# Performance work log

Measured on AMD Instinct MI355X. Metric: run time of the kernel, lower is better.

## Reference

```python
import jax, jax.numpy as jnp
import numpy as np
from jax import lax

K_NBR = 9  # K nearest neighbors
R = 2      # shuffle_scale


def pixel_unshuffle(x, r):
    B, C, H, W = x.shape
    x = x.reshape(B, C, H // r, r, W // r, r)
    return x.transpose(0, 1, 3, 5, 2, 4).reshape(B, C * r * r, H // r, W // r)


def pixel_shuffle(x, r):
    B, C, H, W = x.shape
    x = x.reshape(B, C // (r * r), r, r, H, W)
    return x.transpose(0, 1, 4, 2, 5, 3).reshape(B, C // (r * r), H * r, W * r)


def conv2d_same(x, w, b):
    y = lax.conv_general_dilated(x, w, (1, 1), 'SAME',
                                 dimension_numbers=('NCHW', 'OIHW', 'NCHW'))
    return y + b[None, :, None, None]


def convnn_branching_layer(x, idx, wa, ba, wb, bb, wp, bp):
    """Conv2d_ConvNN_Random_Branching with shuffle_pattern='BA'."""
    x = pixel_unshuffle(x, R)                      # (B, C*r^2, H/r, W/r)
    B, C, H, W = x.shape
    T = H * W
    # Branch 1: standard 3x3 conv
    y1 = conv2d_same(x, wa, ba)                    # (B, c1, H, W)
    # Branch 2: ConvNN on K nearest of N random samples
    xt = x.reshape(B, C, T)                        # tokens
    samp = xt[:, :, idx]                           # (B, C, N) random samples
    dots = jnp.einsum('bct,bcn->btn', xt, samp)
    xn = jnp.sum(xt * xt, axis=1)[:, :, None]      # (B, T, 1)
    sn = jnp.sum(samp * samp, axis=1)[:, None, :]  # (B, 1, N)
    dist = xn + sn - 2.0 * dots                    # squared euclidean (B, T, N)
    nbr = lax.top_k(-dist, K_NBR)[1]               # (B, T, K) indices into samples
    # gather neighbor features: (B, C, T*K)
    g = jnp.take_along_axis(samp, nbr.reshape(B, 1, T * K_NBR), axis=2)
    g = g.reshape(B, C, T, K_NBR)
    # Conv1d(kernel=K, stride=K) over stacked neighbors
    y2 = jnp.einsum('bctk,ock->bot', g, wb) + bb[None, :, None]
    y2 = y2.reshape(B, wb.shape[0], H, W)          # (B, c2, H, W)
    y = jax.nn.relu(jnp.concatenate([y1, y2], axis=1))
    y = conv2d_same(y, wp, bp)                     # 1x1 -> out*r^2 channels
    return pixel_shuffle(y, R)                     # (B, out, H*r, W*r)


def setup_inputs() -> dict:
    key = jax.random.key(0)
    ks = jax.random.split(key, 24)
    s = 0.02
    B = 256
    inp = {
        'x': jax.random.normal(ks[0], (B, 3, 32, 32), jnp.float32),
        'idx1': jax.random.randint(ks[1], (64,), 0, 256, jnp.int32),
        'idx2': jax.random.randint(ks[2], (64,), 0, 256, jnp.int32),
        # layer 1: Cin = 3*4 = 12, branches 16+16, out 16*4 = 64 pre-shuffle
        'w1a': jax.random.normal(ks[3], (16, 12, 3, 3), jnp.float32) * s,
        'b1a': jnp.zeros((16,), jnp.float32),
        'w1b': jax.random.normal(ks[4], (16, 12, 9), jnp.float32) * s,
        'b1b': jnp.zeros((16,), jnp.float32),
        'w1p': jax.random.normal(ks[5], (64, 32, 1, 1), jnp.float32) * s,
        'b1p': jnp.zeros((64,), jnp.float32),
        # layer 2: Cin = 16*4 = 64, branches 32+32, out 32*4 = 128 pre-shuffle
        'w2a': jax.random.normal(ks[6], (32, 64, 3, 3), jnp.float32) * s,
        'b2a': jnp.zeros((32,), jnp.float32),
        'w2b': jax.random.normal(ks[7], (32, 64, 9), jnp.float32) * s,
        'b2b': jnp.zeros((32,), jnp.float32),
        'w2p': jax.random.normal(ks[8], (128, 64, 1, 1), jnp.float32) * s,
        'b2p': jnp.zeros((128,), jnp.float32),
        # FC head
        'fc1w': jax.random.normal(ks[9], (1024, 32768), jnp.float32) * s,
        'fc1b': jnp.zeros((1024,), jnp.float32),
        'fc2w': jax.random.normal(ks[10], (10, 1024), jnp.float32) * s,
        'fc2b': jnp.zeros((10,), jnp.float32),
    }
    return inp


def reference(x, idx1, idx2, w1a, b1a, w1b, b1b, w1p, b1p,
              w2a, b2a, w2b, b2b, w2p, b2p, fc1w, fc1b, fc2w, fc2b):
    h = convnn_branching_layer(x, idx1, w1a, b1a, w1b, b1b, w1p, b1p)  # (B,16,32,32)
    h = convnn_branching_layer(h, idx2, w2a, b2a, w2b, b2b, w2p, b2p)  # (B,32,32,32)
    h = h.reshape(h.shape[0], -1)                   # (B, 32768)
    h = jax.nn.relu(h @ fc1w.T + fc1b)
    return h @ fc2w.T + fc2b                        # (B, num_classes)
```

## Files before the change

### kernel.cpp

```cpp
#include <hip/hip_runtime.h>
#include <cstdint>
#include <cstddef>


#define DI static __device__ __forceinline__

typedef __attribute__((ext_vector_type(8))) short short8;
typedef __attribute__((ext_vector_type(4))) float f32x4;

DI unsigned short f2bf(float v) {
  return __builtin_bit_cast(unsigned short, (__bf16)v);
}
DI float bf2f(unsigned short h) {
  return (float)__builtin_bit_cast(__bf16, h);
}

DI float xu1_at(const float* __restrict__ x, int b, int c, int t) {
  int h = t >> 4, w = t & 15;
  return x[(((size_t)b * 3 + (c >> 2)) * 32 + 2 * h + ((c >> 1) & 1)) * 32 + 2 * w + (c & 1)];
}

__global__ __launch_bounds__(256) void k_prepw(
    const float* __restrict__ w1b, float* __restrict__ wT1,
    const float* __restrict__ w2b, float* __restrict__ wT2,
    const float* __restrict__ w1p, float* __restrict__ wp1T,
    const float* __restrict__ w2p, float* __restrict__ wp2T,
    const float* __restrict__ w1a, float* __restrict__ wa1T,
    const float* __restrict__ w2a, float* __restrict__ wa2T)
{
  int i = blockIdx.x * 256 + threadIdx.x;
  if (i < 1728) {
    int k = i / 192, r = i % 192, c = r >> 4, o = r & 15;
    wT1[i] = w1b[((size_t)o * 12 + c) * 9 + k];
    return;
  }
  i -= 1728;
  if (i < 18432) {
    int k = i / 2048, r = i % 2048, c = r >> 5, o = r & 31;
    wT2[i] = w2b[((size_t)o * 64 + c) * 9 + k];
    return;
  }
  i -= 18432;
  if (i < 2048) { int ic = i >> 6, o = i & 63; wp1T[i] = w1p[(size_t)o * 32 + ic]; return; }
  i -= 2048;
  if (i < 8192) { int ic = i >> 7, o = i & 127; wp2T[i] = w2p[(size_t)o * 64 + ic]; return; }
  i -= 8192;
  if (i < 1728) {
    int o = i & 15, u = i >> 4, ic = u / 9, tp = u % 9;
    wa1T[i] = w1a[((size_t)o * 12 + ic) * 9 + tp];
    return;
  }
  i -= 1728;
  if (i < 18432) {
    int o = i & 31, u = i >> 5, ic = u / 9, tp = u % 9;
    wa2T[i] = w2a[((size_t)o * 64 + ic) * 9 + tp];
  }
}

template <int CIN, bool GATHER, int CCTOT, int OCT>
__global__ __launch_bounds__(256) void k_conv3x3(
    const float* __restrict__ xsrc, const float* __restrict__ xu,
    const float* __restrict__ waT, const float* __restrict__ bias,
    float* __restrict__ ycat)
{
  int b = blockIdx.x;
  int ocb = blockIdx.y * 16;
  __shared__ float xs[CIN * 256];
  int t = threadIdx.x;
  if (GATHER) {
    for (int i = t; i < CIN * 256; i += 256) {
      int c = i >> 8, tt = i & 255;
      xs[i] = xu1_at(xsrc, b, c, tt);
    }
  } else {
    for (int i = t; i < CIN * 256; i += 256) xs[i] = xu[(size_t)b * CIN * 256 + i];
  }
  __syncthreads();
  int tt = t & 127, og = t >> 7;
  int oc0 = ocb + og * 8;
  int h0 = tt >> 4, wc = tt & 15;
  float acc0[8], acc1[8];
#pragma unroll
  for (int o = 0; o < 8; ++o) { acc0[o] = bias[oc0 + o]; acc1[o] = acc0[o]; }
  bool vw0 = wc > 0, vw2 = wc < 15, vh0 = h0 > 0, vh7 = h0 < 7;
  bool m0v[9] = {vh0 && vw0, vh0, vh0 && vw2, vw0, true, vw2, vw0, true, vw2};
  bool m1v[9] = {vw0, true, vw2, vw0, true, vw2, vh7 && vw0, vh7, vh7 && vw2};
  int tc0[9], tc1[9];
#pragma unroll
  for (int dh = 0; dh < 3; ++dh)
#pragma unroll
    for (int dw = 0; dw < 3; ++dw) {
      int o0 = (h0 + dh - 1) * 16 + (wc + dw - 1);
      int o1 = (h0 + 8 + dh - 1) * 16 + (wc + dw - 1);
      tc0[dh * 3 + dw] = o0 < 0 ? 0 : (o0 > 255 ? 255 : o0);
      tc1[dh * 3 + dw] = o1 < 0 ? 0 : (o1 > 255 ? 255 : o1);
    }
#pragma unroll 2
  for (int ic = 0; ic < CIN; ++ic) {
    float xv0[9], xv1[9];
#pragma unroll
    for (int tp = 0; tp < 9; ++tp) {
      float v0 = xs[ic * 256 + tc0[tp]];
      float v1 = xs[ic * 256 + tc1[tp]];
      xv0[tp] = m0v[tp] ? v0 : 0.f;
      xv1[tp] = m1v[tp] ? v1 : 0.f;
    }
#pragma unroll
    for (int tp = 0; tp < 9; ++tp) {
      const float* wp = waT + ((size_t)ic * 9 + tp) * OCT + oc0;
      float4 wA = *(const float4*)wp;
      float4 wB = *(const float4*)(wp + 4);
      float wv[8] = {wA.x, wA.y, wA.z, wA.w, wB.x, wB.y, wB.z, wB.w};
#pragma unroll
      for (int o = 0; o < 8; ++o) {
        acc0[o] = fmaf(xv0[tp], wv[o], acc0[o]);
        acc1[o] = fmaf(xv1[tp], wv[o], acc1[o]);
      }
    }
  }
#pragma unroll
  for (int o = 0; o < 8; ++o) {
    ycat[((size_t)b * CCTOT + oc0 + o) * 256 + tt] = fmaxf(acc0[o], 0.f);
    ycat[((size_t)b * CCTOT + oc0 + o) * 256 + tt + 128] = fmaxf(acc1[o], 0.f);
  }
}

template <int C, int STR, bool GATHER>
__global__ __launch_bounds__(256) void k_prep(
    const float* __restrict__ xsrc, const float* __restrict__ xu,
    const int* __restrict__ idx,
    float* __restrict__ sampT, float* __restrict__ samp_cn,
    float* __restrict__ snvg)
{
  int b = blockIdx.x, t = threadIdx.x;
  __shared__ float sph[C * 64];
  __shared__ int idxs[64];
  if (t < 64) idxs[t] = idx[t];
  __syncthreads();
  for (int i = t; i < C * 64; i += 256) {
    int c = i >> 6, n = i & 63;
    int p = idxs[n];
    sph[i] = GATHER ? xu1_at(xsrc, b, c, p) : xu[((size_t)b * C + c) * 256 + p];
  }
  __syncthreads();
  for (int i = t; i < C * 64; i += 256) samp_cn[(size_t)b * C * 64 + i] = sph[i];
  for (int i = t; i < 64 * STR; i += 256) {
    int n = i / STR, c = i % STR;
    if (c < C) sampT[(size_t)b * 64 * STR + i] = sph[c * 64 + n];
  }
  if (t < 64) {
    float s;
    {
#pragma clang fp contract(off)
      s = 0.f;
      for (int c = 0; c < C; ++c) { float v = sph[c * 64 + t]; s += v * v; }
    }
    snvg[(size_t)b * 64 + t] = s;
  }
}

template <int C, int STR, bool GATHER>
__global__ __launch_bounds__(256) void k_nbr(
    const float* __restrict__ xsrc, const float* __restrict__ xu,
    const float* __restrict__ sampT, const float* __restrict__ snvg,
    int* __restrict__ nbr)
{
  int b = blockIdx.x, t = threadIdx.x;
  float xcol[C];
#pragma unroll
  for (int c = 0; c < C; ++c)
    xcol[c] = GATHER ? xu1_at(xsrc, b, c, t) : xu[((size_t)b * C + c) * 256 + t];
  float xn;
  {
#pragma clang fp contract(off)
    xn = 0.f;
#pragma unroll
    for (int c = 0; c < C; ++c) xn += xcol[c] * xcol[c];
  }
  float bd[9];
  int bn[9];
#pragma unroll
  for (int i = 0; i < 9; ++i) { bd[i] = __builtin_inff(); bn[i] = 1 << 30; }

#pragma unroll 1
  for (int n = 0; n < 64; ++n) {
    const float* sp = sampT + ((size_t)b * 64 + n) * STR;
    float snvn = snvg[(size_t)b * 64 + n];
    float d;
    {
#pragma clang fp contract(off)
      float dot = 0.f;
#pragma unroll
      for (int c = 0; c < C; ++c) dot = fmaf(xcol[c], sp[c], dot);
      d = (xn + snvn) - 2.f * dot;
    }
    if (d < bd[8] || (d == bd[8] && n < bn[8])) {
      float dc = d;
      int nc = n;
#pragma unroll
      for (int i = 0; i < 9; ++i) {
        bool sw = (dc < bd[i]) || (dc == bd[i] && nc < bn[i]);
        float ob = bd[i]; int on = bn[i];
        bd[i] = sw ? dc : ob; bn[i] = sw ? nc : on;
        dc = sw ? ob : dc;   nc = sw ? on : nc;
      }
    }
  }
#pragma unroll
  for (int k = 0; k < 9; ++k) nbr[((size_t)b * 9 + k) * 256 + t] = bn[k];
}

template <int C, int OPT, int OTOT, int CCTOT, int OCBASE>
__global__ __launch_bounds__(256) void k_einsum(
    const float* __restrict__ samp_cn,
    const int* __restrict__ nbr,
    const float* __restrict__ wT,
    const float* __restrict__ bb,
    float* __restrict__ ycat)
{
  int b = blockIdx.x, t = threadIdx.x;
  int tt = t & 127, og = t >> 7;
  int o0 = og * OPT;
  __shared__ float samps[C * 64];
  for (int i = t; i < C * 64; i += 256)
    samps[i] = samp_cn[(size_t)b * C * 64 + i];
  int bnA[9], bnB[9];
#pragma unroll
  for (int k = 0; k < 9; ++k) {
    bnA[k] = nbr[((size_t)b * 9 + k) * 256 + tt];
    bnB[k] = nbr[((size_t)b * 9 + k) * 256 + tt + 128];
  }
  __syncthreads();
  float acc0[OPT], acc1[OPT];
#pragma unroll
  for (int o = 0; o < OPT; ++o) { acc0[o] = bb[o0 + o]; acc1[o] = acc0[o]; }
#pragma unroll 1
  for (int k = 0; k < 9; ++k) {
    int n0 = bnA[k], n1 = bnB[k];
#pragma unroll 2
    for (int c = 0; c < C; ++c) {
      float sv0 = samps[c * 64 + n0];
      float sv1 = samps[c * 64 + n1];
      const float* wp = wT + ((size_t)k * C + c) * OTOT + o0;
#pragma unroll
      for (int oq = 0; oq < OPT / 4; ++oq) {
        float4 wv = ((const float4*)wp)[oq];
        float w4[4] = {wv.x, wv.y, wv.z, wv.w};
#pragma unroll
        for (int j = 0; j < 4; ++j) {
          acc0[oq * 4 + j] = fmaf(sv0, w4[j], acc0[oq * 4 + j]);
          acc1[oq * 4 + j] = fmaf(sv1, w4[j], acc1[oq * 4 + j]);
        }
      }
    }
  }
#pragma unroll
  for (int o = 0; o < OPT; ++o) {
    ycat[((size_t)b * CCTOT + OCBASE + o0 + o) * 256 + tt] = fmaxf(acc0[o], 0.f);
    ycat[((size_t)b * CCTOT + OCBASE + o0 + o) * 256 + tt + 128] = fmaxf(acc1[o], 0.f);
  }
}

template <int CIN, int OPT, int OCTOT, bool SHUF>
__global__ __launch_bounds__(256) void k_conv1x1(
    const float* __restrict__ yin, const float* __restrict__ wpT,
    const float* __restrict__ bias, float* __restrict__ out)
{
  int b = blockIdx.x, ocb = blockIdx.y * 2 * OPT, t = threadIdx.x;
  int tt = t & 127, og = t >> 7;
  int o0 = ocb + og * OPT;
  __shared__ float ys[CIN * 256];
  for (int i = t; i < CIN * 256; i += 256) ys[i] = yin[(size_t)b * CIN * 256 + i];
  __syncthreads();
  float acc0[OPT], acc1[OPT];
#pragma unroll
  for (int o = 0; o < OPT; ++o) { acc0[o] = bias[o0 + o]; acc1[o] = acc0[o]; }
#pragma unroll 2
  for (int ic = 0; ic < CIN; ++ic) {
    float sv0 = ys[ic * 256 + tt];
    float sv1 = ys[ic * 256 + tt + 128];
    const float* wp = wpT + (size_t)ic * OCTOT + o0;
#pragma unroll
    for (int oq = 0; oq < OPT / 4; ++oq) {
      float4 wv = ((const float4*)wp)[oq];
      float w4[4] = {wv.x, wv.y, wv.z, wv.w};
#pragma unroll
      for (int j = 0; j < 4; ++j) {
        acc0[oq * 4 + j] = fmaf(sv0, w4[j], acc0[oq * 4 + j]);
        acc1[oq * 4 + j] = fmaf(sv1, w4[j], acc1[oq * 4 + j]);
      }
    }
  }
  int h0 = tt >> 4, wc = tt & 15;
#pragma unroll
  for (int o = 0; o < OPT; ++o) {
    int ogl = o0 + o;
    if (SHUF) {
      int f0 = (ogl >> 2) * 1024 + (2 * h0 + ((ogl >> 1) & 1)) * 32 + (2 * wc + (ogl & 1));
      int f1 = (ogl >> 2) * 1024 + (2 * (h0 + 8) + ((ogl >> 1) & 1)) * 32 + (2 * wc + (ogl & 1));
      out[(size_t)b * 32768 + f0] = acc0[o];
      out[(size_t)b * 32768 + f1] = acc1[o];
    } else {
      out[((size_t)b * OCTOT + ogl) * 256 + tt] = acc0[o];
      out[((size_t)b * OCTOT + ogl) * 256 + tt + 128] = acc1[o];
    }
  }
}

__global__ __launch_bounds__(256, 2) void k_fc1(
    const float* __restrict__ A, const float* __restrict__ W,
    float* __restrict__ parts)
{
  constexpr int KTOT = 32768;
  constexpr int LDT = 36;
  __shared__ unsigned short Ah[128 * LDT], Am[128 * LDT], Al[128 * LDT];
  int t = threadIdx.x;
  int nb = blockIdx.x, mb = blockIdx.y, sb = blockIdx.z;
  int m0 = mb * 128, n0 = nb * 128, k0 = sb * 1024;
  int wave = t >> 6, lane = t & 63;
  int q = lane >> 4, m16 = lane & 15;

  f32x4 acc[8][2];
#pragma unroll
  for (int mt = 0; mt < 8; ++mt)
#pragma unroll
    for (int nt = 0; nt < 2; ++nt) acc[mt][nt] = (f32x4){0.f, 0.f, 0.f, 0.f};

  int arow = t >> 1, acol = (t & 1) * 16;
  const float* Ap = A + (size_t)(m0 + arow) * KTOT + k0 + acol;
  const float* W0 = W + (size_t)(n0 + wave * 32 + m16) * KTOT + k0 + q * 8;
  const float* W1 = W + (size_t)(n0 + wave * 32 + 16 + m16) * KTOT + k0 + q * 8;

  float4 aR0 = *(const float4*)(Ap + 0);
  float4 aR1 = *(const float4*)(Ap + 4);
  float4 aR2 = *(const float4*)(Ap + 8);
  float4 aR3 = *(const float4*)(Ap + 12);
  float4 w0a = *(const float4*)(W0), w0b = *(const float4*)(W0 + 4);
  float4 w1a = *(const float4*)(W1), w1b = *(const float4*)(W1 + 4);

  for (int ks = 0; ks < 1024; ks += 32) {
    int ksn = (ks + 32 < 1024) ? ks + 32 : 0;
    float4 nA0 = *(const float4*)(Ap + ksn);
    float4 nA1 = *(const float4*)(Ap + ksn + 4);
    float4 nA2 = *(const float4*)(Ap + ksn + 8);
    float4 nA3 = *(const float4*)(Ap + ksn + 12);
    float4 nW0a = *(const float4*)(W0 + ksn), nW0b = *(const float4*)(W0 + ksn + 4);
    float4 nW1a = *(const float4*)(W1 + ksn), nW1b = *(const float4*)(W1 + ksn + 4);

    short8 bh[2], bm[2], bl[2];
    {
      float wf0[8] = {w0a.x, w0a.y, w0a.z, w0a.w, w0b.x, w0b.y, w0b.z, w0b.w};
      float wf1[8] = {w1a.x, w1a.y, w1a.z, w1a.w, w1b.x, w1b.y, w1b.z, w1b.w};
#pragma unroll
      for (int j = 0; j < 8; ++j) {
        unsigned short h = f2bf(wf0[j]); float r1 = wf0[j] - bf2f(h);
        unsigned short m = f2bf(r1);
        bh[0][j] = (short)h; bm[0][j] = (short)m; bl[0][j] = (short)f2bf(r1 - bf2f(m));
        h = f2bf(wf1[j]); r1 = wf1[j] - bf2f(h);
        m = f2bf(r1);
        bh[1][j] = (short)h; bm[1][j] = (short)m; bl[1][j] = (short)f2bf(r1 - bf2f(m));
      }
    }
    short8 vh0, vh1, vm0, vm1, vl0, vl1;
    {
      float av[16] = {aR0.x, aR0.y, aR0.z, aR0.w, aR1.x, aR1.y, aR1.z, aR1.w,
                      aR2.x, aR2.y, aR2.z, aR2.w, aR3.x, aR3.y, aR3.z, aR3.w};
#pragma unroll
      for (int j = 0; j < 8; ++j) {
        {
          float v = av[j];
          unsigned short h = f2bf(v); float r1 = v - bf2f(h);
          unsigned short m = f2bf(r1);
          vh0[j] = (short)h; vm0[j] = (short)m; vl0[j] = (short)f2bf(r1 - bf2f(m));
        }
        {
          float v = av[j + 8];
          unsigned short h = f2bf(v); float r1 = v - bf2f(h);
          unsigned short m = f2bf(r1);
          vh1[j] = (short)h; vm1[j] = (short)m; vl1[j] = (short)f2bf(r1 - bf2f(m));
        }
      }
    }
    __syncthreads();
    {
      int off = arow * LDT + acol;
      *(short8*)&Ah[off] = vh0; *(short8*)&Ah[off + 8] = vh1;
      *(short8*)&Am[off] = vm0; *(short8*)&Am[off + 8] = vm1;
      *(short8*)&Al[off] = vl0; *(short8*)&Al[off + 8] = vl1;
    }
    __syncthreads();
#pragma unroll
    for (int mt = 0; mt < 8; ++mt) {
      int aoff = (mt * 16 + m16) * LDT + q * 8;
      short8 ah = *(const short8*)&Ah[aoff];
      short8 am = *(const short8*)&Am[aoff];
      short8 al = *(const short8*)&Al[aoff];
#pragma unroll
      for (int nt = 0; nt < 2; ++nt) {
        acc[mt][nt] = __builtin_amdgcn_mfma_f32_16x16x32_bf16(al, bh[nt], acc[mt][nt], 0, 0, 0);
        acc[mt][nt] = __builtin_amdgcn_mfma_f32_16x16x32_bf16(am, bm[nt], acc[mt][nt], 0, 0, 0);
        acc[mt][nt] = __builtin_amdgcn_mfma_f32_16x16x32_bf16(ah, bl[nt], acc[mt][nt], 0, 0, 0);
        acc[mt][nt] = __builtin_amdgcn_mfma_f32_16x16x32_bf16(am, bh[nt], acc[mt][nt], 0, 0, 0);
        acc[mt][nt] = __builtin_amdgcn_mfma_f32_16x16x32_bf16(ah, bm[nt], acc[mt][nt], 0, 0, 0);
        acc[mt][nt] = __builtin_amdgcn_mfma_f32_16x16x32_bf16(ah, bh[nt], acc[mt][nt], 0, 0, 0);
      }
    }
    aR0 = nA0; aR1 = nA1; aR2 = nA2; aR3 = nA3;
    w0a = nW0a; w0b = nW0b; w1a = nW1a; w1b = nW1b;
  }
  float* P = parts + (size_t)sb * 262144;
#pragma unroll
  for (int mt = 0; mt < 8; ++mt)
#pragma unroll
    for (int nt = 0; nt < 2; ++nt)
#pragma unroll
      for (int r2 = 0; r2 < 4; ++r2) {
        int m = m0 + mt * 16 + q * 4 + r2;
        int n = n0 + wave * 32 + nt * 16 + m16;
        P[(size_t)m * 1024 + n] = acc[mt][nt][r2];
      }
}

__global__ __launch_bounds__(256) void k_fc1_reduce(const float* __restrict__ parts,
                                                    const float* __restrict__ bias,
                                                    float* __restrict__ h1) {
  int i = blockIdx.x * 256 + threadIdx.x;
  float s = 0.f;
#pragma unroll
  for (int sb = 0; sb < 32; ++sb) s += parts[(size_t)sb * 262144 + i];
  h1[i] = fmaxf(s + bias[i & 1023], 0.f);
}

__global__ __launch_bounds__(256) void k_fc2(const float* __restrict__ h1,
                                             const float* __restrict__ w,
                                             const float* __restrict__ bias,
                                             float* __restrict__ out)
{
  int m = blockIdx.x, tid = threadIdx.x;
  __shared__ float hs[1024];
  __shared__ float ps[256];
  for (int i = tid; i < 1024; i += 256) hs[i] = h1[(size_t)m * 1024 + i];
  __syncthreads();
  int n = tid >> 4, sl = tid & 15;
  float p = 0.f;
  if (n < 10) {
    const float* wr = w + (size_t)n * 1024 + sl * 64;
    const float* hr = hs + sl * 64;
#pragma unroll 8
    for (int j = 0; j < 64; ++j) p = fmaf(hr[j], wr[j], p);
  }
  ps[tid] = p;
  __syncthreads();
  if (sl == 0 && n < 10) {
    float s = 0.f;
#pragma unroll
    for (int q = 0; q < 16; ++q) s += ps[n * 16 + q];
    out[(size_t)m * 10 + n] = s + bias[n];
  }
}

extern "C" void kernel_launch(void* const* d_in, const int* in_sizes, int n_in,
                              void* d_out, int out_size, void* d_ws, size_t ws_size,
                              hipStream_t stream) {
  (void)in_sizes; (void)n_in; (void)out_size; (void)ws_size;
  const float* x    = (const float*)d_in[0];
  const int*   idx1 = (const int*)d_in[1];
  const int*   idx2 = (const int*)d_in[2];
  const float* w1a  = (const float*)d_in[3];
  const float* b1a  = (const float*)d_in[4];
  const float* w1b  = (const float*)d_in[5];
  const float* b1b  = (const float*)d_in[6];
  const float* w1p  = (const float*)d_in[7];
  const float* b1p  = (const float*)d_in[8];
  const float* w2a  = (const float*)d_in[9];
  const float* b2a  = (const float*)d_in[10];
  const float* w2b  = (const float*)d_in[11];
  const float* b2b  = (const float*)d_in[12];
  const float* w2p  = (const float*)d_in[13];
  const float* b2p  = (const float*)d_in[14];
  const float* fc1w = (const float*)d_in[15];
  const float* fc1b = (const float*)d_in[16];
  const float* fc2w = (const float*)d_in[17];
  const float* fc2b = (const float*)d_in[18];

  float* ws    = (float*)d_ws;
  float* xu2   = ws + 0;
  float* ycat1 = ws + 4194304;
  float* ycat2 = ws + 4194304;
  float* WGT   = ws + 8388608;
  float* wT1   = WGT + 0;
  float* wT2   = WGT + 1728;
  float* wp1T  = WGT + 20160;
  float* wp2T  = WGT + 22208;
  float* wa1T  = WGT + 30400;
  float* wa2T  = WGT + 32128;
  float* h1    = ws + 8650752;
  float* hshuf = ws + 10485760;
  float* H        = ws + 10485760;
  int*   nbr      = (int*)(H + 0);
  float* sampT1   = H + 589824;
  float* snv1     = H + 851968;
  float* sampT2   = H + 868352;
  float* snv2     = H + 1916928;
  float* samp_cn1 = H + 1933312;
  float* samp_cn2 = H + 2129920;
  float* parts = ws + 0;
  float* out   = (float*)d_out;

  k_prepw<<<198, 256, 0, stream>>>(w1b, wT1, w2b, wT2, w1p, wp1T, w2p, wp2T, w1a, wa1T, w2a, wa2T);
  k_conv3x3<12, true, 32, 16><<<dim3(256, 1), 256, 0, stream>>>(x, nullptr, wa1T, b1a, ycat1);
  k_prep<12, 16, true><<<256, 256, 0, stream>>>(x, nullptr, idx1, sampT1, samp_cn1, snv1);
  k_nbr<12, 16, true><<<256, 256, 0, stream>>>(x, nullptr, sampT1, snv1, nbr);
  k_einsum<12, 8, 16, 32, 16><<<256, 256, 0, stream>>>(samp_cn1, nbr, wT1, b1b, ycat1);
  k_conv1x1<32, 32, 64, false><<<dim3(256, 1), 256, 0, stream>>>(ycat1, wp1T, b1p, xu2);
  k_conv3x3<64, false, 64, 32><<<dim3(256, 2), 256, 0, stream>>>(nullptr, xu2, wa2T, b2a, ycat2);
  k_prep<64, 64, false><<<256, 256, 0, stream>>>(nullptr, xu2, idx2, sampT2, samp_cn2, snv2);
  k_nbr<64, 64, false><<<256, 256, 0, stream>>>(nullptr, xu2, sampT2, snv2, nbr);
  k_einsum<64, 16, 32, 64, 32><<<256, 256, 0, stream>>>(samp_cn2, nbr, wT2, b2b, ycat2);
  k_conv1x1<64, 32, 128, true><<<dim3(256, 2), 256, 0, stream>>>(ycat2, wp2T, b2p, hshuf);
  k_fc1<<<dim3(8, 2, 32), 256, 0, stream>>>(hshuf, fc1w, parts);
  k_fc1_reduce<<<1024, 256, 0, stream>>>(parts, fc1b, h1);
  k_fc2<<<256, 256, 0, stream>>>(h1, fc2w, fc2b, out);
}
```

Measured before the change: 677.4 us.

## Raise per-block thread counts and split neighbor search across sample groups

The conv3x3, einsum and conv1x1 kernels now use one thread per pixel in blocks of 512 or 1024 threads, instead of two pixels per thread. The conv3x3 and conv1x1 grids drop to a single block per batch. k_nbr splits the 64 samples into four groups of 16 per pixel and merges the partial top-9 lists through shared memory. The aim is more threads in flight and a shorter serial distance loop. The cost is larger blocks, fewer blocks for the grids that lost their second dimension, more shared memory in k_nbr, and a serial merge done only by the first 256 threads.

Result: slower. 782.7 us (+15.6%).

```diff
diff --git a/kernel.cpp b/kernel.cpp
--- a/kernel.cpp
+++ b/kernel.cpp
@@ -58,71 +58,64 @@
 }
 
 template <int CIN, bool GATHER, int CCTOT, int OCT>
-__global__ __launch_bounds__(256) void k_conv3x3(
+__global__ __launch_bounds__(512) void k_conv3x3(
     const float* __restrict__ xsrc, const float* __restrict__ xu,
     const float* __restrict__ waT, const float* __restrict__ bias,
     float* __restrict__ ycat)
 {
+  constexpr int OPT3 = OCT / 2;
   int b = blockIdx.x;
-  int ocb = blockIdx.y * 16;
   __shared__ float xs[CIN * 256];
   int t = threadIdx.x;
   if (GATHER) {
-    for (int i = t; i < CIN * 256; i += 256) {
+    for (int i = t; i < CIN * 256; i += 512) {
       int c = i >> 8, tt = i & 255;
       xs[i] = xu1_at(xsrc, b, c, tt);
     }
   } else {
-    for (int i = t; i < CIN * 256; i += 256) xs[i] = xu[(size_t)b * CIN * 256 + i];
-  }
-  __syncthreads();
-  int tt = t & 127, og = t >> 7;
-  int oc0 = ocb + og * 8;
-  int h0 = tt >> 4, wc = tt & 15;
-  float acc0[8], acc1[8];
-#pragma unroll
-  for (int o = 0; o < 8; ++o) { acc0[o] = bias[oc0 + o]; acc1[o] = acc0[o]; }
-  bool vw0 = wc > 0, vw2 = wc < 15, vh0 = h0 > 0, vh7 = h0 < 7;
-  bool m0v[9] = {vh0 && vw0, vh0, vh0 && vw2, vw0, true, vw2, vw0, true, vw2};
-  bool m1v[9] = {vw0, true, vw2, vw0, true, vw2, vh7 && vw0, vh7, vh7 && vw2};
-  int tc0[9], tc1[9];
+    for (int i = t; i < CIN * 256; i += 512) xs[i] = xu[(size_t)b * CIN * 256 + i];
+  }
+  __syncthreads();
+  int tt = t & 255, og = t >> 8;
+  int oc0 = og * OPT3;
+  int hh = tt >> 4, wc = tt & 15;
+  float acc0[OPT3];
+#pragma unroll
+  for (int o = 0; o < OPT3; ++o) acc0[o] = bias[oc0 + o];
+  bool vw0 = wc > 0, vw2 = wc < 15, vt = hh > 0, vb = hh < 15;
+  bool mv[9] = {vt && vw0, vt, vt && vw2, vw0, true, vw2, vb && vw0, vb, vb && vw2};
+  int tc[9];
 #pragma unroll
   for (int dh = 0; dh < 3; ++dh)
 #pragma unroll
     for (int dw = 0; dw < 3; ++dw) {
-      int o0 = (h0 + dh - 1) * 16 + (wc + dw - 1);
-      int o1 = (h0 + 8 + dh - 1) * 16 + (wc + dw - 1);
-      tc0[dh * 3 + dw] = o0 < 0 ? 0 : (o0 > 255 ? 255 : o0);
-      tc1[dh * 3 + dw] = o1 < 0 ? 0 : (o1 > 255 ? 255 : o1);
+      int o0 = (hh + dh - 1) * 16 + (wc + dw - 1);
+      tc[dh * 3 + dw] = o0 < 0 ? 0 : (o0 > 255 ? 255 : o0);
     }
 #pragma unroll 2
   for (int ic = 0; ic < CIN; ++ic) {
-    float xv0[9], xv1[9];
+    float xv[9];
 #pragma unroll
     for (int tp = 0; tp < 9; ++tp) {
-      float v0 = xs[ic * 256 + tc0[tp]];
-      float v1 = xs[ic * 256 + tc1[tp]];
-      xv0[tp] = m0v[tp] ? v0 : 0.f;
-      xv1[tp] = m1v[tp] ? v1 : 0.f;
+      float v = xs[ic * 256 + tc[tp]];
+      xv[tp] = mv[tp] ? v : 0.f;
     }
 #pragma unroll
     for (int tp = 0; tp < 9; ++tp) {
       const float* wp = waT + ((size_t)ic * 9 + tp) * OCT + oc0;
-      float4 wA = *(const float4*)wp;
-      float4 wB = *(const float4*)(wp + 4);
-      float wv[8] = {wA.x, wA.y, wA.z, wA.w, wB.x, wB.y, wB.z, wB.w};
-#pragma unroll
-      for (int o = 0; o < 8; ++o) {
-        acc0[o] = fmaf(xv0[tp], wv[o], acc0[o]);
-        acc1[o] = fmaf(xv1[tp], wv[o], acc1[o]);
-      }
-    }
-  }
-#pragma unroll
-  for (int o = 0; o < 8; ++o) {
+#pragma unroll
+      for (int oq = 0; oq < OPT3 / 4; ++oq) {
+        float4 wv = ((const float4*)wp)[oq];
+        float w4[4] = {wv.x, wv.y, wv.z, wv.w};
+#pragma unroll
+        for (int j = 0; j < 4; ++j)
+          acc0[oq * 4 + j] = fmaf(xv[tp], w4[j], acc0[oq * 4 + j]);
+      }
+    }
+  }
+#pragma unroll
+  for (int o = 0; o < OPT3; ++o)
     ycat[((size_t)b * CCTOT + oc0 + o) * 256 + tt] = fmaxf(acc0[o], 0.f);
-    ycat[((size_t)b * CCTOT + oc0 + o) * 256 + tt + 128] = fmaxf(acc1[o], 0.f);
-  }
 }
 
 template <int C, int STR, bool GATHER>
@@ -160,16 +153,19 @@
 }
 
 template <int C, int STR, bool GATHER>
-__global__ __launch_bounds__(256) void k_nbr(
+__global__ __launch_bounds__(1024) void k_nbr(
     const float* __restrict__ xsrc, const float* __restrict__ xu,
     const float* __restrict__ sampT, const float* __restrict__ snvg,
     int* __restrict__ nbr)
 {
   int b = blockIdx.x, t = threadIdx.x;
+  int px = t & 255, g = t >> 8;
+  __shared__ float md[4][256][9];
+  __shared__ int mn_[4][256][9];
   float xcol[C];
 #pragma unroll
   for (int c = 0; c < C; ++c)
-    xcol[c] = GATHER ? xu1_at(xsrc, b, c, t) : xu[((size_t)b * C + c) * 256 + t];
+    xcol[c] = GATHER ? xu1_at(xsrc, b, c, px) : xu[((size_t)b * C + c) * 256 + px];
   float xn;
   {
 #pragma clang fp contract(off)
@@ -183,7 +179,7 @@
   for (int i = 0; i < 9; ++i) { bd[i] = __builtin_inff(); bn[i] = 1 << 30; }
 
 #pragma unroll 1
-  for (int n = 0; n < 64; ++n) {
+  for (int n = g * 16; n < g * 16 + 16; ++n) {
     const float* sp = sampT + ((size_t)b * 64 + n) * STR;
     float snvn = snvg[(size_t)b * 64 + n];
     float d;
@@ -207,11 +203,38 @@
     }
   }
 #pragma unroll
-  for (int k = 0; k < 9; ++k) nbr[((size_t)b * 9 + k) * 256 + t] = bn[k];
+  for (int k = 0; k < 9; ++k) { md[g][px][k] = bd[k]; mn_[g][px][k] = bn[k]; }
+  __syncthreads();
+  if (g == 0) {
+    float fd[9];
+    int fn[9];
+#pragma unroll
+    for (int i = 0; i < 9; ++i) { fd[i] = __builtin_inff(); fn[i] = 1 << 30; }
+#pragma unroll 1
+    for (int gg = 0; gg < 4; ++gg)
+#pragma unroll
+      for (int k = 0; k < 9; ++k) {
+        float d = md[gg][px][k];
+        int n = mn_[gg][px][k];
+        if (d < fd[8] || (d == fd[8] && n < fn[8])) {
+          float dc = d;
+          int nc = n;
+#pragma unroll
+          for (int i = 0; i < 9; ++i) {
+            bool sw = (dc < fd[i]) || (dc == fd[i] && nc < fn[i]);
+            float ob = fd[i]; int on = fn[i];
+            fd[i] = sw ? dc : ob; fn[i] = sw ? nc : on;
+            dc = sw ? ob : dc;   nc = sw ? on : nc;
+          }
+        }
+      }
+#pragma unroll
+    for (int k = 0; k < 9; ++k) nbr[((size_t)b * 9 + k) * 256 + px] = fn[k];
+  }
 }
 
 template <int C, int OPT, int OTOT, int CCTOT, int OCBASE>
-__global__ __launch_bounds__(256) void k_einsum(
+__global__ __launch_bounds__(512) void k_einsum(
     const float* __restrict__ samp_cn,
     const int* __restrict__ nbr,
     const float* __restrict__ wT,
@@ -219,76 +242,66 @@
     float* __restrict__ ycat)
 {
   int b = blockIdx.x, t = threadIdx.x;
-  int tt = t & 127, og = t >> 7;
+  int tt = t & 255, og = t >> 8;
   int o0 = og * OPT;
   __shared__ float samps[C * 64];
-  for (int i = t; i < C * 64; i += 256)
+  for (int i = t; i < C * 64; i += 512)
     samps[i] = samp_cn[(size_t)b * C * 64 + i];
-  int bnA[9], bnB[9];
-#pragma unroll
-  for (int k = 0; k < 9; ++k) {
+  int bnA[9];
+#pragma unroll
+  for (int k = 0; k < 9; ++k)
     bnA[k] = nbr[((size_t)b * 9 + k) * 256 + tt];
-    bnB[k] = nbr[((size_t)b * 9 + k) * 256 + tt + 128];
-  }
-  __syncthreads();
-  float acc0[OPT], acc1[OPT];
-#pragma unroll
-  for (int o = 0; o < OPT; ++o) { acc0[o] = bb[o0 + o]; acc1[o] = acc0[o]; }
+  __syncthreads();
+  float acc0[OPT];
+#pragma unroll
+  for (int o = 0; o < OPT; ++o) acc0[o] = bb[o0 + o];
 #pragma unroll 1
   for (int k = 0; k < 9; ++k) {
-    int n0 = bnA[k], n1 = bnB[k];
+    int n0 = bnA[k];
 #pragma unroll 2
     for (int c = 0; c < C; ++c) {
       float sv0 = samps[c * 64 + n0];
-      float sv1 = samps[c * 64 + n1];
       const float* wp = wT + ((size_t)k * C + c) * OTOT + o0;
 #pragma unroll
       for (int oq = 0; oq < OPT / 4; ++oq) {
         float4 wv = ((const float4*)wp)[oq];
         float w4[4] = {wv.x, wv.y, wv.z, wv.w};
 #pragma unroll
-        for (int j = 0; j < 4; ++j) {
+        for (int j = 0; j < 4; ++j)
           acc0[oq * 4 + j] = fmaf(sv0, w4[j], acc0[oq * 4 + j]);
-          acc1[oq * 4 + j] = fmaf(sv1, w4[j], acc1[oq * 4 + j]);
-        }
-      }
-    }
-  }
-#pragma unroll
-  for (int o = 0; o < OPT; ++o) {
+      }
+    }
+  }
+#pragma unroll
+  for (int o = 0; o < OPT; ++o)
     ycat[((size_t)b * CCTOT + OCBASE + o0 + o) * 256 + tt] = fmaxf(acc0[o], 0.f);
-    ycat[((size_t)b * CCTOT + OCBASE + o0 + o) * 256 + tt + 128] = fmaxf(acc1[o], 0.f);
-  }
 }
 
 template <int CIN, int OPT, int OCTOT, bool SHUF>
-__global__ __launch_bounds__(256) void k_conv1x1(
+__global__ __launch_bounds__(1024) void k_conv1x1(
     const float* __restrict__ yin, const float* __restrict__ wpT,
     const float* __restrict__ bias, float* __restrict__ out)
 {
-  int b = blockIdx.x, ocb = blockIdx.y * 2 * OPT, t = threadIdx.x;
-  int tt = t & 127, og = t >> 7;
-  int o0 = ocb + og * OPT;
+  int b = blockIdx.x, t = threadIdx.x;
+  int tt = t & 255, og = t >> 8;
+  int o0 = og * OPT;
   __shared__ float ys[CIN * 256];
-  for (int i = t; i < CIN * 256; i += 256) ys[i] = yin[(size_t)b * CIN * 256 + i];
-  __syncthreads();
-  float acc0[OPT], acc1[OPT];
-#pragma unroll
-  for (int o = 0; o < OPT; ++o) { acc0[o] = bias[o0 + o]; acc1[o] = acc0[o]; }
+  for (int i = t; i < CIN * 256; i += 1024) ys[i] = yin[(size_t)b * CIN * 256 + i];
+  __syncthreads();
+  float acc0[OPT];
+#pragma unroll
+  for (int o = 0; o < OPT; ++o) acc0[o] = bias[o0 + o];
 #pragma unroll 2
   for (int ic = 0; ic < CIN; ++ic) {
     float sv0 = ys[ic * 256 + tt];
-    float sv1 = ys[ic * 256 + tt + 128];
     const float* wp = wpT + (size_t)ic * OCTOT + o0;
 #pragma unroll
     for (int oq = 0; oq < OPT / 4; ++oq) {
       float4 wv = ((const float4*)wp)[oq];
       float w4[4] = {wv.x, wv.y, wv.z, wv.w};
 #pragma unroll
-      for (int j = 0; j < 4; ++j) {
+      for (int j = 0; j < 4; ++j)
         acc0[oq * 4 + j] = fmaf(sv0, w4[j], acc0[oq * 4 + j]);
-        acc1[oq * 4 + j] = fmaf(sv1, w4[j], acc1[oq * 4 + j]);
-      }
     }
   }
   int h0 = tt >> 4, wc = tt & 15;
@@ -297,12 +310,9 @@
     int ogl = o0 + o;
     if (SHUF) {
       int f0 = (ogl >> 2) * 1024 + (2 * h0 + ((ogl >> 1) & 1)) * 32 + (2 * wc + (ogl & 1));
-      int f1 = (ogl >> 2) * 1024 + (2 * (h0 + 8) + ((ogl >> 1) & 1)) * 32 + (2 * wc + (ogl & 1));
       out[(size_t)b * 32768 + f0] = acc0[o];
-      out[(size_t)b * 32768 + f1] = acc1[o];
     } else {
       out[((size_t)b * OCTOT + ogl) * 256 + tt] = acc0[o];
-      out[((size_t)b * OCTOT + ogl) * 256 + tt + 128] = acc1[o];
     }
   }
 }
@@ -508,16 +518,16 @@
   float* out   = (float*)d_out;
 
   k_prepw<<<198, 256, 0, stream>>>(w1b, wT1, w2b, wT2, w1p, wp1T, w2p, wp2T, w1a, wa1T, w2a, wa2T);
-  k_conv3x3<12, true, 32, 16><<<dim3(256, 1), 256, 0, stream>>>(x, nullptr, wa1T, b1a, ycat1);
+  k_conv3x3<12, true, 32, 16><<<256, 512, 0, stream>>>(x, nullptr, wa1T, b1a, ycat1);
   k_prep<12, 16, true><<<256, 256, 0, stream>>>(x, nullptr, idx1, sampT1, samp_cn1, snv1);
-  k_nbr<12, 16, true><<<256, 256, 0, stream>>>(x, nullptr, sampT1, snv1, nbr);
-  k_einsum<12, 8, 16, 32, 16><<<256, 256, 0, stream>>>(samp_cn1, nbr, wT1, b1b, ycat1);
-  k_conv1x1<32, 32, 64, false><<<dim3(256, 1), 256, 0, stream>>>(ycat1, wp1T, b1p, xu2);
-  k_conv3x3<64, false, 64, 32><<<dim3(256, 2), 256, 0, stream>>>(nullptr, xu2, wa2T, b2a, ycat2);
+  k_nbr<12, 16, true><<<256, 1024, 0, stream>>>(x, nullptr, sampT1, snv1, nbr);
+  k_einsum<12, 8, 16, 32, 16><<<256, 512, 0, stream>>>(samp_cn1, nbr, wT1, b1b, ycat1);
+  k_conv1x1<32, 16, 64, false><<<256, 1024, 0, stream>>>(ycat1, wp1T, b1p, xu2);
+  k_conv3x3<64, false, 64, 32><<<256, 512, 0, stream>>>(nullptr, xu2, wa2T, b2a, ycat2);
   k_prep<64, 64, false><<<256, 256, 0, stream>>>(nullptr, xu2, idx2, sampT2, samp_cn2, snv2);
-  k_nbr<64, 64, false><<<256, 256, 0, stream>>>(nullptr, xu2, sampT2, snv2, nbr);
-  k_einsum<64, 16, 32, 64, 32><<<256, 256, 0, stream>>>(samp_cn2, nbr, wT2, b2b, ycat2);
-  k_conv1x1<64, 32, 128, true><<<dim3(256, 2), 256, 0, stream>>>(ycat2, wp2T, b2p, hshuf);
+  k_nbr<64, 64, false><<<256, 1024, 0, stream>>>(nullptr, xu2, sampT2, snv2, nbr);
+  k_einsum<64, 16, 32, 64, 32><<<256, 512, 0, stream>>>(samp_cn2, nbr, wT2, b2b, ycat2);
+  k_conv1x1<64, 32, 128, true><<<256, 1024, 0, stream>>>(ycat2, wp2T, b2p, hshuf);
   k_fc1<<<dim3(8, 2, 32), 256, 0, stream>>>(hshuf, fc1w, parts);
   k_fc1_reduce<<<1024, 256, 0, stream>>>(parts, fc1b, h1);
   k_fc2<<<256, 256, 0, stream>>>(h1, fc2w, fc2b, out);
```

## Fuse sample prep, KNN search and neighbor einsum into one kernel per layer

Applied to the files above, without the earlier changes.

Merges the three kernels (sample gather/norms, nearest-neighbor top-k, and neighbor conv1d einsum) into a single per-batch kernel that keeps the sampled features, their norms and the neighbor indices in shared memory. This removes two launches per layer and the global round-trips for sampT, samp_cn, snv and nbr. The cost is higher shared-memory use per block (C*64 floats plus 9*256 ints), which may lower occupancy, and the dot-product loop now reads samples from LDS broadcast instead of global/cache.

New measurement: 648.2 us. 4.3% less time.

```diff
diff --git a/kernel.cpp b/kernel.cpp
--- a/kernel.cpp
+++ b/kernel.cpp
@@ -125,16 +125,19 @@
   }
 }
 
-template <int C, int STR, bool GATHER>
-__global__ __launch_bounds__(256) void k_prep(
+template <int C, bool GATHER, int OPT, int OTOT, int CCTOT, int OCBASE>
+__global__ __launch_bounds__(256) void k_knn(
     const float* __restrict__ xsrc, const float* __restrict__ xu,
     const int* __restrict__ idx,
-    float* __restrict__ sampT, float* __restrict__ samp_cn,
-    float* __restrict__ snvg)
+    const float* __restrict__ wT,
+    const float* __restrict__ bb,
+    float* __restrict__ ycat)
 {
   int b = blockIdx.x, t = threadIdx.x;
   __shared__ float sph[C * 64];
+  __shared__ float snvs[64];
   __shared__ int idxs[64];
+  __shared__ int nbs[9 * 256];
   if (t < 64) idxs[t] = idx[t];
   __syncthreads();
   for (int i = t; i < C * 64; i += 256) {
@@ -143,11 +146,6 @@
     sph[i] = GATHER ? xu1_at(xsrc, b, c, p) : xu[((size_t)b * C + c) * 256 + p];
   }
   __syncthreads();
-  for (int i = t; i < C * 64; i += 256) samp_cn[(size_t)b * C * 64 + i] = sph[i];
-  for (int i = t; i < 64 * STR; i += 256) {
-    int n = i / STR, c = i % STR;
-    if (c < C) sampT[(size_t)b * 64 * STR + i] = sph[c * 64 + n];
-  }
   if (t < 64) {
     float s;
     {
@@ -155,17 +153,8 @@
       s = 0.f;
       for (int c = 0; c < C; ++c) { float v = sph[c * 64 + t]; s += v * v; }
     }
-    snvg[(size_t)b * 64 + t] = s;
-  }
-}
-
-template <int C, int STR, bool GATHER>
-__global__ __launch_bounds__(256) void k_nbr(
-    const float* __restrict__ xsrc, const float* __restrict__ xu,
-    const float* __restrict__ sampT, const float* __restrict__ snvg,
-    int* __restrict__ nbr)
-{
-  int b = blockIdx.x, t = threadIdx.x;
+    snvs[t] = s;
+  }
   float xcol[C];
 #pragma unroll
   for (int c = 0; c < C; ++c)
@@ -177,21 +166,20 @@
 #pragma unroll
     for (int c = 0; c < C; ++c) xn += xcol[c] * xcol[c];
   }
+  __syncthreads();
   float bd[9];
   int bn[9];
 #pragma unroll
   for (int i = 0; i < 9; ++i) { bd[i] = __builtin_inff(); bn[i] = 1 << 30; }
-
 #pragma unroll 1
   for (int n = 0; n < 64; ++n) {
-    const float* sp = sampT + ((size_t)b * 64 + n) * STR;
-    float snvn = snvg[(size_t)b * 64 + n];
+    float snvn = snvs[n];
     float d;
     {
 #pragma clang fp contract(off)
       float dot = 0.f;
 #pragma unroll
-      for (int c = 0; c < C; ++c) dot = fmaf(xcol[c], sp[c], dot);
+      for (int c = 0; c < C; ++c) dot = fmaf(xcol[c], sph[c * 64 + n], dot);
       d = (xn + snvn) - 2.f * dot;
     }
     if (d < bd[8] || (d == bd[8] && n < bn[8])) {
@@ -207,30 +195,16 @@
     }
   }
 #pragma unroll
-  for (int k = 0; k < 9; ++k) nbr[((size_t)b * 9 + k) * 256 + t] = bn[k];
-}
-
-template <int C, int OPT, int OTOT, int CCTOT, int OCBASE>
-__global__ __launch_bounds__(256) void k_einsum(
-    const float* __restrict__ samp_cn,
-    const int* __restrict__ nbr,
-    const float* __restrict__ wT,
-    const float* __restrict__ bb,
-    float* __restrict__ ycat)
-{
-  int b = blockIdx.x, t = threadIdx.x;
+  for (int k = 0; k < 9; ++k) nbs[k * 256 + t] = bn[k];
+  __syncthreads();
   int tt = t & 127, og = t >> 7;
   int o0 = og * OPT;
-  __shared__ float samps[C * 64];
-  for (int i = t; i < C * 64; i += 256)
-    samps[i] = samp_cn[(size_t)b * C * 64 + i];
   int bnA[9], bnB[9];
 #pragma unroll
   for (int k = 0; k < 9; ++k) {
-    bnA[k] = nbr[((size_t)b * 9 + k) * 256 + tt];
-    bnB[k] = nbr[((size_t)b * 9 + k) * 256 + tt + 128];
-  }
-  __syncthreads();
+    bnA[k] = nbs[k * 256 + tt];
+    bnB[k] = nbs[k * 256 + tt + 128];
+  }
   float acc0[OPT], acc1[OPT];
 #pragma unroll
   for (int o = 0; o < OPT; ++o) { acc0[o] = bb[o0 + o]; acc1[o] = acc0[o]; }
@@ -239,8 +213,8 @@
     int n0 = bnA[k], n1 = bnB[k];
 #pragma unroll 2
     for (int c = 0; c < C; ++c) {
-      float sv0 = samps[c * 64 + n0];
-      float sv1 = samps[c * 64 + n1];
+      float sv0 = sph[c * 64 + n0];
+      float sv1 = sph[c * 64 + n1];
       const float* wp = wT + ((size_t)k * C + c) * OTOT + o0;
 #pragma unroll
       for (int oq = 0; oq < OPT / 4; ++oq) {
@@ -496,27 +470,15 @@
   float* wa2T  = WGT + 32128;
   float* h1    = ws + 8650752;
   float* hshuf = ws + 10485760;
-  float* H        = ws + 10485760;
-  int*   nbr      = (int*)(H + 0);
-  float* sampT1   = H + 589824;
-  float* snv1     = H + 851968;
-  float* sampT2   = H + 868352;
-  float* snv2     = H + 1916928;
-  float* samp_cn1 = H + 1933312;
-  float* samp_cn2 = H + 2129920;
   float* parts = ws + 0;
   float* out   = (float*)d_out;
 
   k_prepw<<<198, 256, 0, stream>>>(w1b, wT1, w2b, wT2, w1p, wp1T, w2p, wp2T, w1a, wa1T, w2a, wa2T);
   k_conv3x3<12, true, 32, 16><<<dim3(256, 1), 256, 0, stream>>>(x, nullptr, wa1T, b1a, ycat1);
-  k_prep<12, 16, true><<<256, 256, 0, stream>>>(x, nullptr, idx1, sampT1, samp_cn1, snv1);
-  k_nbr<12, 16, true><<<256, 256, 0, stream>>>(x, nullptr, sampT1, snv1, nbr);
-  k_einsum<12, 8, 16, 32, 16><<<256, 256, 0, stream>>>(samp_cn1, nbr, wT1, b1b, ycat1);
+  k_knn<12, true, 8, 16, 32, 16><<<256, 256, 0, stream>>>(x, nullptr, idx1, wT1, b1b, ycat1);
   k_conv1x1<32, 32, 64, false><<<dim3(256, 1), 256, 0, stream>>>(ycat1, wp1T, b1p, xu2);
   k_conv3x3<64, false, 64, 32><<<dim3(256, 2), 256, 0, stream>>>(nullptr, xu2, wa2T, b2a, ycat2);
-  k_prep<64, 64, false><<<256, 256, 0, stream>>>(nullptr, xu2, idx2, sampT2, samp_cn2, snv2);
-  k_nbr<64, 64, false><<<256, 256, 0, stream>>>(nullptr, xu2, sampT2, snv2, nbr);
-  k_einsum<64, 16, 32, 64, 32><<<256, 256, 0, stream>>>(samp_cn2, nbr, wT2, b2b, ycat2);
+  k_knn<64, false, 16, 32, 64, 32><<<256, 256, 0, stream>>>(nullptr, xu2, idx2, wT2, b2b, ycat2);
   k_conv1x1<64, 32, 128, true><<<dim3(256, 2), 256, 0, stream>>>(ycat2, wp2T, b2p, hshuf);
   k_fc1<<<dim3(8, 2, 32), 256, 0, stream>>>(hshuf, fc1w, parts);
   k_fc1_reduce<<<1024, 256, 0, stream>>>(parts, fc1b, h1);
```
